# Optimization experiments

Measured on AMD Instinct MI355X. Metric: run time of the kernel, lower is better.

Reference implementation:

```python
import jax, jax.numpy as jnp
import numpy as np

D_MODEL = 1024
N_HEADS = 16
HEAD_DIM = D_MODEL // N_HEADS
D_FF = 4096
BATCH = 4
SEQ = 2048
LN_EPS = 1e-5


def layer_norm(x, g, b):
    mu = jnp.mean(x, axis=-1, keepdims=True)
    var = jnp.mean(jnp.square(x - mu), axis=-1, keepdims=True)
    return (x - mu) * jax.lax.rsqrt(var + LN_EPS) * g + b


def setup_inputs() -> dict:
    key = jax.random.key(0)
    ks = jax.random.split(key, 8)
    s = 0.02
    x = jax.random.normal(ks[0], (BATCH, SEQ, D_MODEL), jnp.float32)
    mask = jnp.triu(jnp.ones((SEQ, SEQ), dtype=bool), k=1)  # True = masked
    return {
        "x": x,
        "ln1_g": jnp.ones((D_MODEL,), jnp.float32),
        "ln1_b": jnp.zeros((D_MODEL,), jnp.float32),
        "qkv_w": jax.random.normal(ks[1], (3 * D_MODEL, D_MODEL), jnp.float32) * s,
        "qkv_b": jnp.zeros((3 * D_MODEL,), jnp.float32),
        "out_w": jax.random.normal(ks[2], (D_MODEL, D_MODEL), jnp.float32) * s,
        "out_b": jnp.zeros((D_MODEL,), jnp.float32),
        "ln2_g": jnp.ones((D_MODEL,), jnp.float32),
        "ln2_b": jnp.zeros((D_MODEL,), jnp.float32),
        "fc1_w": jax.random.normal(ks[3], (D_FF, D_MODEL), jnp.float32) * s,
        "fc1_b": jnp.zeros((D_FF,), jnp.float32),
        "fc2_w": jax.random.normal(ks[4], (D_MODEL, D_FF), jnp.float32) * s,
        "fc2_b": jnp.zeros((D_MODEL,), jnp.float32),
        "mask": mask,
    }


def reference(x, ln1_g, ln1_b, qkv_w, qkv_b, out_w, out_b,
              ln2_g, ln2_b, fc1_w, fc1_b, fc2_w, fc2_b, mask):
    b, s, _ = x.shape
    # --- pre-norm attention ---
    h = layer_norm(x, ln1_g, ln1_b)
    qkv = h @ qkv_w.T + qkv_b                       # [b, s, 3*D]
    qkv = qkv.reshape(b, s, 3, N_HEADS, HEAD_DIM)
    q, k, v = (jnp.moveaxis(qkv[:, :, i], 2, 1) for i in range(3))  # [b, H, s, hd]
    scale = HEAD_DIM ** -0.5
    attn = jnp.einsum('bhqd,bhkd->bhqk', q, k) * scale
    attn = jnp.where(mask, -jnp.inf, attn)
    attn = jax.nn.softmax(attn, axis=-1)
    o = jnp.einsum('bhqk,bhkd->bhqd', attn, v)      # [b, H, s, hd]
    o = jnp.moveaxis(o, 1, 2).reshape(b, s, D_MODEL)
    x = x + (o @ out_w.T + out_b)
    # --- pre-norm FFN ---
    h = layer_norm(x, ln2_g, ln2_b)
    h = jax.nn.gelu(h @ fc1_w.T + fc1_b, approximate=False)
    x = x + (h @ fc2_w.T + fc2_b)
    return x
```

## Files before the change

kernel.cpp:

```cpp
#include <hip/hip_runtime.h>
#include <math.h>

using u16 = unsigned short;
typedef __attribute__((ext_vector_type(8))) short short8;
typedef __attribute__((ext_vector_type(4))) float f32x4;
typedef __attribute__((ext_vector_type(16))) float f32x16;
typedef __attribute__((ext_vector_type(4))) u16 u16x4;

#define DEV __device__ __forceinline__

DEV u16 f2bf(float f) {
    unsigned u = __float_as_uint(f);
    u += 0x7fffu + ((u >> 16) & 1u);
    return (u16)(u >> 16);
}
DEV float bf2f(u16 h) { return __uint_as_float(((unsigned)h) << 16); }

DEV short8 ld16(const u16* p) { return *reinterpret_cast<const short8*>(p); }

DEV float gelu_f(float x) {
    const float u = x * (0.7978845608f + 0.0356774081f * x * x);
    const float e = __builtin_amdgcn_exp2f(u * 2.885390082f);
    const float t = 1.f - 2.f * __builtin_amdgcn_rcpf(e + 1.f);
    return 0.5f * x * (1.f + t);
}

DEV unsigned pk2(float a, float b) {
    unsigned r;
    asm("v_cvt_pk_bf16_f32 %0, %1, %2" : "=v"(r) : "v"(a), "v"(b));
    return r;
}

#define GLL16(gp, lp)                                                          \
    __builtin_amdgcn_global_load_lds(                                          \
        (const __attribute__((address_space(1))) void*)(gp),                   \
        (__attribute__((address_space(3))) void*)(lp), 16, 0, 0)

#define VMC(n) asm volatile("s_waitcnt vmcnt(" #n ")" ::: "memory")
#define LGKM0() asm volatile("s_waitcnt lgkmcnt(0)" ::: "memory")

__global__ __launch_bounds__(256) void cvt_all(
    const float* __restrict__ s0, const float* __restrict__ s1,
    const float* __restrict__ s2, const float* __restrict__ s3,
    u16* __restrict__ d0, u16* __restrict__ d1,
    u16* __restrict__ d2, u16* __restrict__ d3) {
    for (long i = (long)blockIdx.x * 256 + threadIdx.x; i < 3145728;
         i += (long)gridDim.x * 256) {
        const float* s; u16* d; long j = i;
        if (j < 786432)       { s = s0; d = d0; }
        else if (j < 1048576) { s = s1; d = d1; j -= 786432; }
        else if (j < 2097152) { s = s2; d = d2; j -= 1048576; }
        else                  { s = s3; d = d3; j -= 2097152; }
        float4 v = reinterpret_cast<const float4*>(s)[j];
        u16x4 o;
        o.x = f2bf(v.x); o.y = f2bf(v.y); o.z = f2bf(v.z); o.w = f2bf(v.w);
        reinterpret_cast<u16x4*>(d)[j] = o;
    }
}

__global__ __launch_bounds__(256) void ln_bf16(const float* __restrict__ x,
                                               const float* __restrict__ gm,
                                               const float* __restrict__ bt,
                                               u16* __restrict__ out) {
    const int row = blockIdx.x, tid = threadIdx.x;
    const float4 v = reinterpret_cast<const float4*>(x + (long)row * 1024)[tid];
    float s  = v.x + v.y + v.z + v.w;
    float sq = v.x * v.x + v.y * v.y + v.z * v.z + v.w * v.w;
#pragma unroll
    for (int off = 1; off <= 32; off <<= 1) {
        s  += __shfl_xor(s, off);
        sq += __shfl_xor(sq, off);
    }
    __shared__ float ss[4], ssq[4];
    const int wave = tid >> 6, lane = tid & 63;
    if (lane == 0) { ss[wave] = s; ssq[wave] = sq; }
    __syncthreads();
    s  = ss[0] + ss[1] + ss[2] + ss[3];
    sq = ssq[0] + ssq[1] + ssq[2] + ssq[3];
    const float mu   = s * (1.f / 1024.f);
    const float var  = sq * (1.f / 1024.f) - mu * mu;
    const float rstd = rsqrtf(var + 1e-5f);
    const float4 g4 = reinterpret_cast<const float4*>(gm)[tid];
    const float4 b4 = reinterpret_cast<const float4*>(bt)[tid];
    u16x4 o;
    o.x = f2bf((v.x - mu) * rstd * g4.x + b4.x);
    o.y = f2bf((v.y - mu) * rstd * g4.y + b4.y);
    o.z = f2bf((v.z - mu) * rstd * g4.z + b4.z);
    o.w = f2bf((v.w - mu) * rstd * g4.w + b4.w);
    reinterpret_cast<u16x4*>(out + (long)row * 1024)[tid] = o;
}

#define TS(c, r) ((c) * 128 + (((((r) >> 3) ^ ((c) & 15))) << 3) + ((r) & 7))
#define CS(r, ck) ((r) * 128 + ((((ck) ^ ((r) & 15))) << 3))

template <int EPI, int BK>
__global__ __launch_bounds__(256, (BK == 32) ? 4 : 2) void gemm_bt(
    const u16* __restrict__ A, const u16* __restrict__ B,
    const float* __restrict__ bias, const float* res, float* outf,
    u16* __restrict__ outb, u16* __restrict__ Qb, u16* __restrict__ Kb,
    u16* __restrict__ Vtb, int M, int N, int K, int ldk) {
    constexpr int BUFU = (BK == 32) ? 8192 : 16384;
    __shared__ u16 shpool[2 * BUFU];

    const int tid = threadIdx.x;
    const int wave = tid >> 6, lane = tid & 63;
    const int lo = lane & 15, g = lane >> 4;
    const int wr = wave >> 1, wc = wave & 1;

    const int nwg = gridDim.x, chunk = nwg >> 3;
    const int wgid = (blockIdx.x & 7) * chunk + (blockIdx.x >> 3);
    const int nSmCol = N >> 10;
    const int s = wgid >> 6, w6 = wgid & 63;
    const int bm = (s / nSmCol) * 8 + (w6 >> 3);
    const int bn = (s % nSmCol) * 8 + (w6 & 7);
    const int row0 = bm * 128, col0 = bn * 128;

    const u16 *Ag, *Bg;
    if constexpr (BK == 32) {
        const int lrow = lane >> 2;
        const int lg   = (lane & 3) ^ ((lane >> 3) & 3);
        Ag = A + (long)(row0 + wave * 16 + lrow) * ldk + lg * 8;
        Bg = B + (long)(col0 + wave * 16 + lrow) * ldk + lg * 8;
    } else {
        const int lg = (lane & 7) ^ ((lane >> 3) & 7);
        Ag = A + (long)(row0 + wave * 32 + (lane >> 3)) * ldk + lg * 8;
        Bg = B + (long)(col0 + wave * 32 + (lane >> 3)) * ldk + lg * 8;
    }

    auto STAGE = [&](int tb, int kt) {
        if constexpr (BK == 32) {
            u16* Al = shpool + tb * 8192 + wave * 512;
            u16* Bl = Al + 4096;
            GLL16(Ag + (long)kt * 32, Al);
            GLL16(Ag + 64 * (long)ldk + (long)kt * 32, Al + 2048);
            GLL16(Bg + (long)kt * 32, Bl);
            GLL16(Bg + 64 * (long)ldk + (long)kt * 32, Bl + 2048);
        } else {
            u16* Al = shpool + tb * 16384 + wave * 2048;
            u16* Bl = Al + 8192;
            GLL16(Ag + (long)kt * 64,                  Al);
            GLL16(Ag + (long)kt * 64 +  8 * (long)ldk, Al + 512);
            GLL16(Ag + (long)kt * 64 + 16 * (long)ldk, Al + 1024);
            GLL16(Ag + (long)kt * 64 + 24 * (long)ldk, Al + 1536);
            GLL16(Bg + (long)kt * 64,                  Bl);
            GLL16(Bg + (long)kt * 64 +  8 * (long)ldk, Bl + 512);
            GLL16(Bg + (long)kt * 64 + 16 * (long)ldk, Bl + 1024);
            GLL16(Bg + (long)kt * 64 + 24 * (long)ldk, Bl + 1536);
        }
    };

    f32x4 acc[4][4] = {};

    STAGE(0, 0);
    STAGE(1, 1);

    const int T = K / BK;
    for (int t = 0; t < T; ++t) {
        const int cur = t & 1;
        if (t + 1 < T) {
            if constexpr (BK == 32) { VMC(4); } else { VMC(8); }
        } else { VMC(0); }
        __builtin_amdgcn_s_barrier();
        const u16* As = shpool + cur * BUFU;
        const u16* Bs = As + BUFU / 2;
        if constexpr (BK == 32) {
            short8 af[4], bfr[4];
            const int agp = g ^ ((lo >> 1) & 3);
#pragma unroll
            for (int m = 0; m < 4; ++m)
                af[m] = ld16(&As[(wr * 64 + m * 16 + lo) * 32 + agp * 8]);
#pragma unroll
            for (int n = 0; n < 4; ++n)
                bfr[n] = ld16(&Bs[(wc * 64 + n * 16 + lo) * 32 + agp * 8]);
            LGKM0();
            __builtin_amdgcn_s_barrier();
            if (t + 2 < T) STAGE(cur, t + 2);
#pragma unroll
            for (int m = 0; m < 4; ++m)
#pragma unroll
                for (int n = 0; n < 4; ++n)
                    acc[m][n] = __builtin_amdgcn_mfma_f32_16x16x32_bf16(
                        bfr[n], af[m], acc[m][n], 0, 0, 0);
        } else {
            short8 af[2][4], bfr[2][4];
#pragma unroll
            for (int ks = 0; ks < 2; ++ks) {
                const int ch = ((ks * 4 + g) ^ (lo & 7)) * 8;
#pragma unroll
                for (int m = 0; m < 4; ++m)
                    af[ks][m] = ld16(&As[(wr * 64 + m * 16 + lo) * 64 + ch]);
#pragma unroll
                for (int n = 0; n < 4; ++n)
                    bfr[ks][n] = ld16(&Bs[(wc * 64 + n * 16 + lo) * 64 + ch]);
            }
            LGKM0();
            __builtin_amdgcn_s_barrier();
            if (t + 2 < T) STAGE(cur, t + 2);
#pragma unroll
            for (int ks = 0; ks < 2; ++ks)
#pragma unroll
                for (int m = 0; m < 4; ++m)
#pragma unroll
                    for (int n = 0; n < 4; ++n)
                        acc[m][n] = __builtin_amdgcn_mfma_f32_16x16x32_bf16(
                            bfr[ks][n], af[ks][m], acc[m][n], 0, 0, 0);
        }
    }

    if constexpr (EPI == 1) {
#pragma unroll
        for (int n = 0; n < 4; ++n) {
            const int cb = col0 + wc * 64 + n * 16 + g * 4;
            const float4 b4 = *reinterpret_cast<const float4*>(&bias[cb]);
#pragma unroll
            for (int m = 0; m < 4; ++m) {
                const int r = row0 + wr * 64 + m * 16 + lo;
                u16x4 o = {f2bf(gelu_f(acc[m][n][0] + b4.x)),
                           f2bf(gelu_f(acc[m][n][1] + b4.y)),
                           f2bf(gelu_f(acc[m][n][2] + b4.z)),
                           f2bf(gelu_f(acc[m][n][3] + b4.w))};
                *reinterpret_cast<u16x4*>(&outb[(long)r * N + cb]) = o;
            }
        }
        return;
    }

    if constexpr (EPI == 3) {
        __syncthreads();
        const int part = col0 >> 10;
        if (part == 2) {
#pragma unroll
            for (int n = 0; n < 4; ++n) {
                const int cb = wc * 64 + n * 16 + g * 4;
                const float4 b4 = *reinterpret_cast<const float4*>(&bias[col0 + cb]);
#pragma unroll
                for (int m = 0; m < 4; ++m) {
                    const int rl = wr * 64 + m * 16 + lo;
                    shpool[TS(cb + 0, rl)] = f2bf(acc[m][n][0] + b4.x);
                    shpool[TS(cb + 1, rl)] = f2bf(acc[m][n][1] + b4.y);
                    shpool[TS(cb + 2, rl)] = f2bf(acc[m][n][2] + b4.z);
                    shpool[TS(cb + 3, rl)] = f2bf(acc[m][n][3] + b4.w);
                }
            }
            __syncthreads();
            const int c = tid >> 1, hlf = tid & 1;
            const int dcol = (col0 - 2048) + c;
            const int head = dcol >> 6, d = dcol & 63;
            const int bb = row0 >> 11;
            u16* dst = Vtb + ((long)(bb * 16 + head) * 64 + d) * 2048 +
                       (row0 & 2047) + hlf * 64;
            const u16* srcb = shpool + c * 128;
#pragma unroll
            for (int i = 0; i < 8; ++i) {
                const int pc = (hlf * 8 + i) ^ (c & 15);
                *reinterpret_cast<short8*>(dst + i * 8) =
                    *reinterpret_cast<const short8*>(srcb + pc * 8);
            }
            return;
        }
        const float qs = (part == 0) ? 0.18033688f : 1.0f;
#pragma unroll
        for (int n = 0; n < 4; ++n) {
            const int cb = col0 + wc * 64 + n * 16 + g * 4;
            const float4 b4 = *reinterpret_cast<const float4*>(&bias[cb]);
            const int ch = wc * 8 + n * 2 + (g >> 1);
#pragma unroll
            for (int m = 0; m < 4; ++m) {
                const int r = wr * 64 + m * 16 + lo;
                u16x4 o = {f2bf((acc[m][n][0] + b4.x) * qs),
                           f2bf((acc[m][n][1] + b4.y) * qs),
                           f2bf((acc[m][n][2] + b4.z) * qs),
                           f2bf((acc[m][n][3] + b4.w) * qs)};
                *reinterpret_cast<u16x4*>(&shpool[CS(r, ch) + (g & 1) * 4]) = o;
            }
        }
        __syncthreads();
        const int row = tid >> 1, hl = tid & 1;
        const int headbase = (col0 & 1023) >> 6;
        const int head = headbase + hl;
        const int bb = row0 >> 11;
        const int srow = (row0 & 2047) + row;
        u16* drow = (part == 0 ? Qb : Kb) +
                    ((long)(bb * 16 + head) * 2048 + srow) * 64;
        const int rk = row & 15;
#pragma unroll
        for (int i = 0; i < 8; ++i) {
            const int ck = hl * 8 + i;
            *reinterpret_cast<short8*>(drow + i * 8) =
                *reinterpret_cast<const short8*>(&shpool[row * 128 + ((ck ^ rk) << 3)]);
        }
        return;
    }

#pragma unroll
    for (int n = 0; n < 4; ++n) {
        const int cb = col0 + wc * 64 + n * 16 + g * 4;
        const float4 b4 = *reinterpret_cast<const float4*>(&bias[cb]);
#pragma unroll
        for (int m = 0; m < 4; ++m) {
            const int r = row0 + wr * 64 + m * 16 + lo;
            const float4 rr = *reinterpret_cast<const float4*>(&res[(long)r * N + cb]);
            float4 o = {rr.x + acc[m][n][0] + b4.x, rr.y + acc[m][n][1] + b4.y,
                        rr.z + acc[m][n][2] + b4.z, rr.w + acc[m][n][3] + b4.w};
            *reinterpret_cast<float4*>(&outf[(long)r * N + cb]) = o;
        }
    }
}

__global__ __launch_bounds__(256) void attn_fwd32(
    const u16* __restrict__ Q, const u16* __restrict__ K,
    const u16* __restrict__ Vt, u16* __restrict__ O) {
    __shared__ u16 kvl[2][8192];
    const int bh = blockIdx.x;
    const int strip = 15 - blockIdx.y;
    const int wave = threadIdx.x >> 6, lane = threadIdx.x & 63;
    const int lq = lane & 31, hi = lane >> 5;
    const int qw = strip * 128 + wave * 32;

    const u16* Kg = K + (long)bh * 2048 * 64;
    const u16* Vg = Vt + (long)bh * 64 * 2048;
    const int bb = bh >> 4, h = bh & 15;
    const u16* Qp = Q + ((long)bh * 2048 + qw) * 64;

    const int srow = wave * 8 + (lane >> 3);
    const int sc   = (lane & 7) ^ (srow & 7);

#define ASTAGE(b, kt) do {                                                     \
        const long kvb = (long)(kt) * 64;                                      \
        GLL16(Kg + (kvb + srow) * 64 + sc * 8,        &kvl[b][wave * 512]);    \
        GLL16(Kg + (kvb + 32 + srow) * 64 + sc * 8,   &kvl[b][2048 + wave * 512]); \
        GLL16(Vg + (long)srow * 2048 + kvb + sc * 8,  &kvl[b][4096 + wave * 512]); \
        GLL16(Vg + (long)(32 + srow) * 2048 + kvb + sc * 8,                    \
              &kvl[b][6144 + wave * 512]);                                     \
    } while (0)

    short8 qf[4];
#pragma unroll
    for (int ks = 0; ks < 4; ++ks)
        qf[ks] = ld16(Qp + lq * 64 + ks * 16 + hi * 8);

    f32x16 o0 = {}, o1 = {};
    float m = -1e30f, l = 0.f;
    const int q_abs = qw + lq;
    const int my_end = qw + 32;
    const int T = 2 * (strip + 1);
    const int swp = lq & 7;

    ASTAGE(0, 0);
    ASTAGE(1, 1);

    for (int t = 0; t < T; ++t) {
        const int cur = t & 1;
        const int kv0 = t * 64;
        if (t + 1 < T) { VMC(4); } else { VMC(0); }
        __builtin_amdgcn_s_barrier();
        const bool active = (kv0 < my_end);
        f32x16 s0 = {}, s1 = {};
        short8 vf0[4], vf1[4];
        if (active) {
            const u16* Kb = &kvl[cur][0];
            __builtin_amdgcn_s_setprio(1);
#pragma unroll
            for (int ks = 0; ks < 4; ++ks)
                s0 = __builtin_amdgcn_mfma_f32_32x32x16_bf16(
                    ld16(Kb + lq * 64 + ((ks * 2 + hi) ^ swp) * 8), qf[ks], s0, 0, 0, 0);
#pragma unroll
            for (int ks = 0; ks < 4; ++ks)
                s1 = __builtin_amdgcn_mfma_f32_32x32x16_bf16(
                    ld16(Kb + 2048 + lq * 64 + ((ks * 2 + hi) ^ swp) * 8), qf[ks], s1, 0, 0, 0);
            __builtin_amdgcn_s_setprio(0);
            const u16* Vb = &kvl[cur][4096];
#pragma unroll
            for (int c = 0; c < 4; ++c) {
                vf0[c] = ld16(Vb + lq * 64 + ((c * 2 + hi) ^ swp) * 8);
                vf1[c] = ld16(Vb + 2048 + lq * 64 + ((c * 2 + hi) ^ swp) * 8);
            }
        }
        LGKM0();
        __builtin_amdgcn_s_barrier();
        if (t + 2 < T) ASTAGE(cur, t + 2);
        if (active) {
            float mt = -1e30f;
            if (kv0 + 64 >= my_end) {
#pragma unroll
                for (int r = 0; r < 16; ++r) {
                    const int kv = kv0 + (r & 3) + 8 * (r >> 2) + 4 * hi;
                    if (kv > q_abs) s0[r] = -1e30f;
                    mt = fmaxf(mt, s0[r]);
                    if (kv + 32 > q_abs) s1[r] = -1e30f;
                    mt = fmaxf(mt, s1[r]);
                }
            } else {
#pragma unroll
                for (int r = 0; r < 16; ++r)
                    mt = fmaxf(mt, fmaxf(s0[r], s1[r]));
            }
            mt = fmaxf(mt, __shfl_xor(mt, 32));

            if (!__all(mt <= m + 11.5f)) {
                const float mn = fmaxf(m, mt);
                const float corr = __builtin_amdgcn_exp2f(m - mn);
                m = mn;
                l *= corr;
                o0 *= corr; o1 *= corr;
            }
            float ps = 0.f;
#pragma unroll
            for (int r = 0; r < 16; ++r) {
                s0[r] = __builtin_amdgcn_exp2f(s0[r] - m); ps += s0[r];
                s1[r] = __builtin_amdgcn_exp2f(s1[r] - m); ps += s1[r];
            }
            l += ps;

            short8 pf[4];
#pragma unroll
            for (int c = 0; c < 4; ++c) {
                const f32x16& src = (c >> 1) ? s1 : s0;
                const int b = (c & 1) * 8;
                const unsigned A0 = pk2(src[b + 0], src[b + 1]);
                const unsigned A1 = pk2(src[b + 2], src[b + 3]);
                const unsigned B0 = pk2(src[b + 4], src[b + 5]);
                const unsigned B1 = pk2(src[b + 6], src[b + 7]);
                const unsigned S0 = hi ? A0 : B0;
                const unsigned S1 = hi ? A1 : B1;
                const unsigned R0 = (unsigned)__shfl_xor((int)S0, 32);
                const unsigned R1 = (unsigned)__shfl_xor((int)S1, 32);
                union { unsigned u[4]; short8 v; } fr;
                fr.u[0] = hi ? R0 : A0;
                fr.u[1] = hi ? R1 : A1;
                fr.u[2] = hi ? B0 : R0;
                fr.u[3] = hi ? B1 : R1;
                pf[c] = fr.v;
            }

            __builtin_amdgcn_s_setprio(1);
#pragma unroll
            for (int c = 0; c < 4; ++c) {
                o0 = __builtin_amdgcn_mfma_f32_32x32x16_bf16(
                    vf0[c], pf[c], o0, 0, 0, 0);
                o1 = __builtin_amdgcn_mfma_f32_32x32x16_bf16(
                    vf1[c], pf[c], o1, 0, 0, 0);
            }
            __builtin_amdgcn_s_setprio(0);
        }
    }
#undef ASTAGE

    l += __shfl_xor(l, 32);
    const float inv = 1.f / l;
    u16* Orow = O + ((long)(bb * 2048 + qw + lq)) * 1024 + h * 64;
#pragma unroll
    for (int k4 = 0; k4 < 4; ++k4) {
        u16x4 w0, w1;
#pragma unroll
        for (int j = 0; j < 4; ++j) {
            w0[j] = f2bf(o0[k4 * 4 + j] * inv);
            w1[j] = f2bf(o1[k4 * 4 + j] * inv);
        }
        *reinterpret_cast<u16x4*>(Orow + 8 * k4 + 4 * hi)      = w0;
        *reinterpret_cast<u16x4*>(Orow + 32 + 8 * k4 + 4 * hi) = w1;
    }
}

extern "C" void kernel_launch(void* const* d_in, const int* in_sizes, int n_in,
                              void* d_out, int out_size, void* d_ws, size_t ws_size,
                              hipStream_t stream) {
    const float* x      = (const float*)d_in[0];
    const float* ln1_g  = (const float*)d_in[1];
    const float* ln1_b  = (const float*)d_in[2];
    const float* qkv_w  = (const float*)d_in[3];
    const float* qkv_b  = (const float*)d_in[4];
    const float* out_w  = (const float*)d_in[5];
    const float* out_b  = (const float*)d_in[6];
    const float* ln2_g  = (const float*)d_in[7];
    const float* ln2_b  = (const float*)d_in[8];
    const float* fc1_w  = (const float*)d_in[9];
    const float* fc1_b  = (const float*)d_in[10];
    const float* fc2_w  = (const float*)d_in[11];
    const float* fc2_b  = (const float*)d_in[12];
    float* out = (float*)d_out;

    const size_t MB = 1024ull * 1024ull;
    if (ws_size < 120 * MB) return;
    char* ws = (char*)d_ws;
    u16* wqkv = (u16*)(ws + 0);
    u16* wout = (u16*)(ws + 6 * MB);
    u16* wfc1 = (u16*)(ws + 8 * MB);
    u16* wfc2 = (u16*)(ws + 16 * MB);
    u16* hbuf = (u16*)(ws + 24 * MB);
    u16* obuf = (u16*)(ws + 40 * MB);
    u16* Qb   = (u16*)(ws + 56 * MB);
    u16* Kb   = (u16*)(ws + 72 * MB);
    u16* Vtb  = (u16*)(ws + 88 * MB);
    u16* gbuf = (u16*)(ws + 56 * MB);

    cvt_all<<<dim3(2048), 256, 0, stream>>>(qkv_w, out_w, fc1_w, fc2_w,
                                            wqkv, wout, wfc1, wfc2);

    ln_bf16<<<8192, 256, 0, stream>>>(x, ln1_g, ln1_b, hbuf);
    gemm_bt<3, 32><<<dim3(1536), 256, 0, stream>>>(hbuf, wqkv, qkv_b, nullptr,
                                                   nullptr, nullptr, Qb, Kb, Vtb,
                                                   8192, 3072, 1024, 1024);
    attn_fwd32<<<dim3(64, 16), 256, 0, stream>>>(Qb, Kb, Vtb, obuf);
    gemm_bt<2, 64><<<dim3(512), 256, 0, stream>>>(obuf, wout, out_b, x, out,
                                                  nullptr, nullptr, nullptr, nullptr,
                                                  8192, 1024, 1024, 1024);
    ln_bf16<<<8192, 256, 0, stream>>>(out, ln2_g, ln2_b, hbuf);
    gemm_bt<1, 32><<<dim3(2048), 256, 0, stream>>>(hbuf, wfc1, fc1_b, nullptr,
                                                   nullptr, gbuf, nullptr, nullptr,
                                                   nullptr, 8192, 4096, 1024, 1024);
    gemm_bt<2, 64><<<dim3(512), 256, 0, stream>>>(gbuf, wfc2, fc2_b, out, out,
                                                  nullptr, nullptr, nullptr, nullptr,
                                                  8192, 1024, 4096, 4096);
}
```

Before: 364.1 us.

## Add dedicated 128x256-tile FC1 GEMM kernel with 8 waves and XCD-aware mapping

Replaces the generic 128x128 gemm_bt FC1 launch with a specialized kernel using 512 threads (8 waves), 128x256 output tiles, and a workgroup remapping that groups blocks per XCD and into super-tiles for L2 reuse. The larger tile raises arithmetic intensity per LDS load and halves the number of workgroups, while the grid remap improves cache locality of A/B panels. This trades more LDS per block (48KB) and possibly lower occupancy for the added reuse, and it hardcodes shape assumptions such as N being a multiple of 1024.

```diff
diff --git a/kernel.cpp b/kernel.cpp
--- a/kernel.cpp
+++ b/kernel.cpp
@@ -88,6 +88,85 @@
     o.z = f2bf((v.z - mu) * rstd * g4.z + b4.z);
     o.w = f2bf((v.w - mu) * rstd * g4.w + b4.w);
     reinterpret_cast<u16x4*>(out + (long)row * 1024)[tid] = o;
+}
+
+__global__ __launch_bounds__(512, 6) void gemm_fc1(
+    const u16* __restrict__ A, const u16* __restrict__ B,
+    const float* __restrict__ bias, u16* __restrict__ outb,
+    int M, int N, int K, int ldk) {
+    __shared__ u16 shpool[24576];
+
+    const int tid = threadIdx.x;
+    const int w = tid >> 6, lane = tid & 63;
+    const int lo = lane & 15, g = lane >> 4;
+    const int wr = w >> 2, wc = w & 3;
+
+    const int nwg = gridDim.x, chunk = nwg >> 3;
+    const int wgid = (blockIdx.x & 7) * chunk + (blockIdx.x >> 3);
+    const int nSmCol = N >> 10;
+    const int s = wgid >> 5, w5 = wgid & 31;
+    const int bm = (s / nSmCol) * 8 + (w5 >> 2);
+    const int bn = (s % nSmCol) * 4 + (w5 & 3);
+    const int row0 = bm * 128, col0 = bn * 256;
+
+    const int lrow = lane >> 2;
+    const int lg   = (lane & 3) ^ ((lane >> 3) & 3);
+    const u16* Ag = A + (long)(row0 + w * 16 + lrow) * ldk + lg * 8;
+    const u16* Bg = B + (long)(col0 + w * 32 + lrow) * ldk + lg * 8;
+
+    auto STAGE = [&](int tb, int kt) {
+        u16* Al = shpool + tb * 12288 + w * 512;
+        u16* Bl = shpool + tb * 12288 + 4096 + w * 1024;
+        GLL16(Ag + (long)kt * 32, Al);
+        GLL16(Bg + (long)kt * 32, Bl);
+        GLL16(Bg + 16 * (long)ldk + (long)kt * 32, Bl + 512);
+    };
+
+    const int agp = g ^ ((lo >> 1) & 3);
+    f32x4 acc[4][4] = {};
+
+    STAGE(0, 0);
+    STAGE(1, 1);
+
+    const int T = K >> 5;
+    for (int t = 0; t < T; ++t) {
+        const int cur = t & 1;
+        if (t + 1 < T) { VMC(3); } else { VMC(0); }
+        __builtin_amdgcn_s_barrier();
+        const u16* As = shpool + cur * 12288;
+        const u16* Bs = As + 4096;
+        short8 af[4], bfr[4];
+#pragma unroll
+        for (int m = 0; m < 4; ++m)
+            af[m] = ld16(&As[(wr * 64 + m * 16 + lo) * 32 + agp * 8]);
+#pragma unroll
+        for (int n = 0; n < 4; ++n)
+            bfr[n] = ld16(&Bs[(wc * 64 + n * 16 + lo) * 32 + agp * 8]);
+        LGKM0();
+        __builtin_amdgcn_s_barrier();
+        if (t + 2 < T) STAGE(cur, t + 2);
+#pragma unroll
+        for (int m = 0; m < 4; ++m)
+#pragma unroll
+            for (int n = 0; n < 4; ++n)
+                acc[m][n] = __builtin_amdgcn_mfma_f32_16x16x32_bf16(
+                    bfr[n], af[m], acc[m][n], 0, 0, 0);
+    }
+
+#pragma unroll
+    for (int n = 0; n < 4; ++n) {
+        const int cb = col0 + wc * 64 + n * 16 + g * 4;
+        const float4 b4 = *reinterpret_cast<const float4*>(&bias[cb]);
+#pragma unroll
+        for (int m = 0; m < 4; ++m) {
+            const int r = row0 + wr * 64 + m * 16 + lo;
+            u16x4 o = {f2bf(gelu_f(acc[m][n][0] + b4.x)),
+                       f2bf(gelu_f(acc[m][n][1] + b4.y)),
+                       f2bf(gelu_f(acc[m][n][2] + b4.z)),
+                       f2bf(gelu_f(acc[m][n][3] + b4.w))};
+            *reinterpret_cast<u16x4*>(&outb[(long)r * N + cb]) = o;
+        }
+    }
 }
 
 #define TS(c, r) ((c) * 128 + (((((r) >> 3) ^ ((c) & 15))) << 3) + ((r) & 7))
@@ -207,24 +286,6 @@
         }
     }
 
-    if constexpr (EPI == 1) {
-#pragma unroll
-        for (int n = 0; n < 4; ++n) {
-            const int cb = col0 + wc * 64 + n * 16 + g * 4;
-            const float4 b4 = *reinterpret_cast<const float4*>(&bias[cb]);
-#pragma unroll
-            for (int m = 0; m < 4; ++m) {
-                const int r = row0 + wr * 64 + m * 16 + lo;
-                u16x4 o = {f2bf(gelu_f(acc[m][n][0] + b4.x)),
-                           f2bf(gelu_f(acc[m][n][1] + b4.y)),
-                           f2bf(gelu_f(acc[m][n][2] + b4.z)),
-                           f2bf(gelu_f(acc[m][n][3] + b4.w))};
-                *reinterpret_cast<u16x4*>(&outb[(long)r * N + cb]) = o;
-            }
-        }
-        return;
-    }
-
     if constexpr (EPI == 3) {
         __syncthreads();
         const int part = col0 >> 10;
@@ -506,9 +567,8 @@
                                                   nullptr, nullptr, nullptr, nullptr,
                                                   8192, 1024, 1024, 1024);
     ln_bf16<<<8192, 256, 0, stream>>>(out, ln2_g, ln2_b, hbuf);
-    gemm_bt<1, 32><<<dim3(2048), 256, 0, stream>>>(hbuf, wfc1, fc1_b, nullptr,
-                                                   nullptr, gbuf, nullptr, nullptr,
-                                                   nullptr, 8192, 4096, 1024, 1024);
+    gemm_fc1<<<dim3(1024), 512, 0, stream>>>(hbuf, wfc1, fc1_b, gbuf,
+                                             8192, 4096, 1024, 1024);
     gemm_bt<2, 64><<<dim3(512), 256, 0, stream>>>(gbuf, wfc2, fc2_b, out, out,
                                                   nullptr, nullptr, nullptr, nullptr,
                                                   8192, 1024, 4096, 4096);
```

Result: slower. 851.9 us (+134.0%).
